# Kernel tuning notes

Hardware: AMD Instinct MI355X
Metric: run time of the kernel (lower is better)

The kernel has to match this reference:

```python
import jax, jax.numpy as jnp
import numpy as np
import math

B_GRAPHS = 256
L_NODES = 64
N_NODES = B_GRAPHS * L_NODES
N_EDGES = N_NODES * 4
HEADS = 8
D_INNER = 512
N_DAGS = 1
DIAMETER = 64


def setup_inputs() -> dict:
    key = jax.random.key(0)
    ks = jax.random.split(key, 8)
    x = jax.random.normal(ks[0], (N_NODES, D_INNER), jnp.float32)
    B = jax.random.normal(ks[1], (N_NODES, D_INNER), jnp.float32)
    C = jax.random.normal(ks[2], (N_NODES, D_INNER), jnp.float32)
    dt = jax.random.normal(ks[3], (N_NODES, N_DAGS * HEADS * 2), jnp.float32)
    dt_edge = jax.random.normal(ks[4], (N_EDGES, N_DAGS * HEADS), jnp.float32)
    # DAG edges: within each graph, src_local < dst_local (gap 1..7) -> strictly upper triangular
    u = jax.random.randint(ks[5], (N_EDGES,), 0, L_NODES - 1)
    gap = jax.random.randint(ks[6], (N_EDGES,), 1, 8)
    v = jnp.minimum(u + gap, L_NODES - 1)
    graph = jnp.arange(N_EDGES) // (N_EDGES // B_GRAPHS)
    edge_index = jnp.stack([graph * L_NODES + u, graph * L_NODES + v]).astype(jnp.int32)
    data_batch = (jnp.arange(N_NODES) // L_NODES).astype(jnp.int32)
    dag_masks = jnp.ones((N_DAGS, N_EDGES), jnp.float32)
    # dt_bias init as in module __init__ (inverse softplus of dt in [1e-3, 1e-1])
    rng = np.random.default_rng(0)
    dtv = np.exp(rng.uniform(size=(HEADS,)) * (math.log(0.1) - math.log(0.001)) + math.log(0.001))
    dtv = np.clip(dtv, 1e-4, None)
    dt_bias = jnp.asarray(dtv + np.log(-np.expm1(-dtv)), jnp.float32)
    D = jnp.ones((HEADS,), jnp.float32)
    return dict(x=x, B=B, C=C, dt=dt, dt_edge=dt_edge, dt_bias=dt_bias, D=D,
                dag_masks=dag_masks, edge_index=edge_index, data_batch=data_batch,
                diameter=DIAMETER)


def _repeated_squaring_inverse(A, diam):
    # (I - A)^{-1} = prod_k (I + A^{2^k}) for nilpotent A; O(log diam) matmuls
    j = 2 ** int(math.ceil(math.log2(diam)))
    I = jnp.eye(A.shape[-1], dtype=A.dtype)
    last = A
    M = I + A
    for _ in range(2, int(math.log2(j)) + 1):
        last = last @ last
        M = M @ (I + last)
    return M


def reference(x, B, C, dt, dt_edge, dt_bias, D, dag_masks, edge_index, data_batch, diameter):
    N, din = x.shape
    g, E = dag_masks.shape
    n = dt_bias.shape[0]
    b = int(data_batch[-1]) + 1
    l = N // b  # equal-size graphs -> dense batching is a reshape, mask all-True
    h = din // n
    src, dst = edge_index[0], edge_index[1]

    # dt_node: (N, g*n*c) -> (c, g, n, N); softplus(dt + bias)
    c = dt.shape[1] // (g * n)
    dtn = dt.reshape(N, g, n, c).transpose(3, 1, 2, 0)
    dtn = jax.nn.softplus(dtn + dt_bias[None, None, :, None])
    dte = dt_edge.reshape(E, g, n).transpose(1, 2, 0)  # (g,n,E)
    dte = jax.nn.softplus(dte + dt_bias[None, :, None])

    dt_s, dt_t = dtn[0], dtn[1]
    dt_sum = (dt_s[:, :, src] + dt_t[:, :, dst] + dte) / np.sqrt(3.0)  # (g,n,E)
    dt_exp = jnp.exp(-dt_sum)
    msk = dag_masks[:, None, :]
    dt_sum = dt_sum * msk
    dt_exp = dt_exp * msk

    # dense adjacency with per-edge attrs; note 'b l1 l2 (g n) -> b g n l2 l1' transpose
    b_e = src // l
    sl = src % l
    dl = dst % l
    attr = dt_exp.transpose(2, 0, 1).reshape(E, g * n)
    adj = jnp.zeros((b, l, l, g * n), x.dtype).at[b_e, sl, dl].add(attr)
    A = adj.reshape(b, l, l, g, n).transpose(0, 3, 4, 2, 1)  # (b,g,n,l,l)

    # normalize_mat: sqrt outer product of in-degree counts, clamped at 1
    ec = jnp.zeros((g, N), x.dtype).at[:, dst].add(dag_masks)
    ec_dense = ec.T.reshape(b, l, g)
    outer = jnp.sqrt(jnp.einsum('blg,btg->bglt', ec_dense, ec_dense))
    outer = jnp.where(outer < 1.0, 1.0, outer)
    A = A / outer[:, :, None]

    dnorm = jnp.zeros((g, n, N), x.dtype).at[:, :, dst].add(dt_sum)
    dnorm = dnorm.transpose(2, 0, 1).reshape(b, l, g, n).transpose(0, 2, 3, 1)  # (b,g,n,l)

    A2 = A.reshape(b, g * n, l, l).astype(jnp.float32)
    L = _repeated_squaring_inverse(A2, int(diameter))
    L = L.reshape(b, g, n, l, l) * dnorm[..., None]

    x4 = x.reshape(b, l, n, h).transpose(0, 2, 1, 3)  # (b,n,l,h)
    B3 = B.reshape(b, l, -1)
    C3 = C.reshape(b, l, -1)
    # y = einsum(C,L,B,x) with B/C broadcast over (g,n): fold C.B^T into L
    CB = jnp.einsum('bld,btd->blt', C3, B3)
    M = L * CB[:, None, None]
    y = jnp.einsum('bgnlt,bnth->bgnlh', M, x4)
    y = y + x4[:, None] * D[None, None, :, None, None]
    y = y.transpose(0, 3, 1, 2, 4).reshape(N, g, n * h)  # b g n l h -> (N, g, n*h)
    y = y.sum(axis=1) / np.sqrt(g)
    return y
```

## Files before the change

kernel.cpp:

```cpp
#include <hip/hip_runtime.h>
#include <math.h>

#define NGRAPH 256
#define LNODE  64
#define HEADS  8
#define DIN    512
#define EPG    256
#define NEDGE  65536

typedef short bf16x8 __attribute__((ext_vector_type(8)));
typedef float f32x4 __attribute__((ext_vector_type(4)));

__device__ __forceinline__ float softplusf(float v) {
    return (v > 20.f) ? v : log1pf(expf(v));
}
__device__ __forceinline__ unsigned short f2bf(float f) {
    union { float f; unsigned u; } c; c.f = f;
    unsigned r = c.u + 0x7fffu + ((c.u >> 16) & 1u);
    return (unsigned short)(r >> 16);
}
__device__ __forceinline__ float bf2f(unsigned short h) {
    union { float f; unsigned u; } c; c.u = ((unsigned)h) << 16;
    return c.f;
}

__global__ __launch_bounds__(256) void cb_kernel(const float* __restrict__ Bm,
                                                 const float* __restrict__ Cm,
                                                 float* __restrict__ CBp,
                                                 int dper, int tposed) {
    int b = blockIdx.x;
    int slice = blockIdx.y;
    __shared__ float Cs[64 * 68];
    __shared__ float Bs[64 * 68];
    int tid = threadIdx.x;
    int ti = tid >> 4, tj = tid & 15;
    float acc[4][4] = {};
    const float* Cg = Cm + (size_t)b * 64 * DIN;
    const float* Bg = Bm + (size_t)b * 64 * DIN;
    int d_lo = slice * dper;
    for (int d0 = d_lo; d0 < d_lo + dper; d0 += 64) {
        __syncthreads();
        #pragma unroll
        for (int k = 0; k < 4; ++k) {
            int f = k * 256 + tid;
            int row = f >> 4;
            int c4 = (f & 15) << 2;
            *(float4*)(Cs + row * 68 + c4) = *(const float4*)(Cg + row * DIN + d0 + c4);
            *(float4*)(Bs + row * 68 + c4) = *(const float4*)(Bg + row * DIN + d0 + c4);
        }
        __syncthreads();
        for (int d = 0; d < 64; d += 4) {
            float4 cr[4], br[4];
            #pragma unroll
            for (int r = 0; r < 4; ++r) cr[r] = *(const float4*)(Cs + (4 * ti + r) * 68 + d);
            #pragma unroll
            for (int c = 0; c < 4; ++c) br[c] = *(const float4*)(Bs + (4 * tj + c) * 68 + d);
            #pragma unroll
            for (int r = 0; r < 4; ++r)
                #pragma unroll
                for (int c = 0; c < 4; ++c)
                    acc[r][c] += cr[r].x * br[c].x + cr[r].y * br[c].y +
                                 cr[r].z * br[c].z + cr[r].w * br[c].w;
        }
    }
    float* outp = CBp + ((size_t)slice * NGRAPH + b) * 4096;
    if (!tposed) {
        #pragma unroll
        for (int r = 0; r < 4; ++r)
            *(float4*)(outp + (4 * ti + r) * 64 + 4 * tj) =
                make_float4(acc[r][0], acc[r][1], acc[r][2], acc[r][3]);
    } else {
        #pragma unroll
        for (int r = 0; r < 4; ++r)
            #pragma unroll
            for (int c = 0; c < 4; ++c)
                outp[(4 * tj + c) * 64 + (4 * ti + r)] = acc[r][c];
    }
}

__global__ __launch_bounds__(256, 4) void fused2_kernel(const float* __restrict__ x,
                                                        const float* __restrict__ dt,
                                                        const float* __restrict__ dt_edge,
                                                        const float* __restrict__ dt_bias,
                                                        const float* __restrict__ Dp,
                                                        const float* __restrict__ dag_masks,
                                                        const int* __restrict__ edge_index,
                                                        const float* __restrict__ CBp,
                                                        float* __restrict__ out,
                                                        int nslice) {
    int b = blockIdx.x;
    int head = blockIdx.y;
    __shared__ unsigned short CBsh[64 * 64];
    __shared__ unsigned short Wl[64 * 72];
    __shared__ unsigned short Xt[64 * 72];
    __shared__ float Ab[512];
    __shared__ float dnsh[64];
    __shared__ float ecsh[64];
    __shared__ float dts[64];
    __shared__ float dtt[64];
    int tid = threadIdx.x;
    int w = tid >> 6;
    int lane = tid & 63;

    for (int s4 = tid; s4 < 1024; s4 += 256) {
        float4 v = make_float4(0.f, 0.f, 0.f, 0.f);
        for (int s = 0; s < nslice; ++s) {
            float4 p = *(const float4*)(CBp + ((size_t)s * NGRAPH + b) * 4096 + s4 * 4);
            v.x += p.x; v.y += p.y; v.z += p.z; v.w += p.w;
        }
        unsigned short* q = &CBsh[s4 * 4];
        q[0] = f2bf(v.x); q[1] = f2bf(v.y); q[2] = f2bf(v.z); q[3] = f2bf(v.w);
    }
    const float* xg0 = x + (size_t)b * 64 * DIN + head * 64;
    #pragma unroll
    for (int k = 0; k < 4; ++k) {
        int s = k * 256 + tid;
        int t = s >> 4;
        int e0 = (s & 15) << 2;
        float4 v = *(const float4*)(xg0 + (size_t)t * DIN + e0);
        Xt[(e0 + 0) * 72 + t] = f2bf(v.x);
        Xt[(e0 + 1) * 72 + t] = f2bf(v.y);
        Xt[(e0 + 2) * 72 + t] = f2bf(v.z);
        Xt[(e0 + 3) * 72 + t] = f2bf(v.w);
    }
    for (int k = tid; k < 512; k += 256) Ab[k] = 0.f;
    float bias = dt_bias[head];
    if (tid < 64) {
        dnsh[tid] = 0.f;
        ecsh[tid] = 0.f;
        int node = b * 64 + tid;
        dts[tid] = softplusf(dt[node * 16 + head * 2 + 0] + bias);
        dtt[tid] = softplusf(dt[node * 16 + head * 2 + 1] + bias);
    }
    __syncthreads();

    {
        int e = b * EPG + tid;
        int sl = edge_index[e] & 63;
        int dl = edge_index[NEDGE + e] & 63;
        float mk = dag_masks[e];
        float de = softplusf(dt_edge[e * HEADS + head] + bias);
        float dsum = (dts[sl] + dtt[dl] + de) * 0.57735026918962576451f;
        float dexp = expf(-dsum);
        atomicAdd(&Ab[dl * 8 + (dl - sl)], dexp * mk);
        atomicAdd(&dnsh[dl], dsum * mk);
        atomicAdd(&ecsh[dl], mk);
    }
    __syncthreads();

    for (int k = tid; k < 512; k += 256) {
        int i = k >> 3, d = k & 7;
        int src = i - d;
        if (d >= 1 && src >= 0) {
            float den = sqrtf(ecsh[i] * ecsh[src]);
            if (den < 1.f) den = 1.f;
            Ab[k] = Ab[k] / den;
        }
    }
    __syncthreads();

    if (w == 0) {
        int j = lane;
        float Dh = Dp[head];
        float mwin[7] = {0.f, 0.f, 0.f, 0.f, 0.f, 0.f, 0.f};
        for (int i = 0; i < 64; ++i) {
            float mi = (j == i) ? 1.f : 0.f;
            #pragma unroll
            for (int s = 0; s < 7; ++s) mi += Ab[i * 8 + s + 1] * mwin[s];
            float wv = mi * bf2f(CBsh[i * 64 + j]) * dnsh[i];
            if (j == i) wv += Dh;
            Wl[i * 72 + j] = f2bf(wv);
            #pragma unroll
            for (int s = 6; s > 0; --s) mwin[s] = mwin[s - 1];
            mwin[0] = mi;
        }
    }
    __syncthreads();

    {
        int m = lane & 15;
        int quad = lane >> 4;
        bf16x8 a0 = *(const bf16x8*)(&Wl[(16 * w + m) * 72 + quad * 8]);
        bf16x8 a1 = *(const bf16x8*)(&Wl[(16 * w + m) * 72 + 32 + quad * 8]);
        float* og = out + ((size_t)b * 64) * DIN + head * 64;
        #pragma unroll
        for (int eb = 0; eb < 4; ++eb) {
            bf16x8 b0 = *(const bf16x8*)(&Xt[(eb * 16 + m) * 72 + quad * 8]);
            bf16x8 b1 = *(const bf16x8*)(&Xt[(eb * 16 + m) * 72 + 32 + quad * 8]);
            f32x4 acc = {0.f, 0.f, 0.f, 0.f};
            acc = __builtin_amdgcn_mfma_f32_16x16x32_bf16(a0, b0, acc, 0, 0, 0);
            acc = __builtin_amdgcn_mfma_f32_16x16x32_bf16(a1, b1, acc, 0, 0, 0);
            #pragma unroll
            for (int r = 0; r < 4; ++r) {
                int row = 16 * w + quad * 4 + r;
                og[(size_t)row * DIN + eb * 16 + m] = acc[r];
            }
        }
    }
}

__global__ __launch_bounds__(256, 4) void fused_kernel(const float* __restrict__ x,
                                                       const float* __restrict__ dt,
                                                       const float* __restrict__ dt_edge,
                                                       const float* __restrict__ dt_bias,
                                                       const float* __restrict__ Dp,
                                                       const float* __restrict__ dag_masks,
                                                       const int* __restrict__ edge_index,
                                                       const float* __restrict__ CBt,
                                                       float* __restrict__ out,
                                                       int nslice) {
    int b = blockIdx.x;
    int head = blockIdx.y;
    __shared__ float Ab[64 * 8];
    __shared__ float Mt[64 * 68];
    __shared__ float Xs[64 * 64];
    __shared__ float dnsh[64];
    __shared__ float ecsh[64];
    __shared__ float dts[64];
    __shared__ float dtt[64];
    int tid = threadIdx.x;

    int t4 = tid >> 2;
    int ib = (tid & 3) << 4;
    float4 cbsum[4];
    #pragma unroll
    for (int g = 0; g < 4; ++g) cbsum[g] = make_float4(0.f, 0.f, 0.f, 0.f);
    for (int s = 0; s < nslice; ++s) {
        const float* p = CBt + ((size_t)s * NGRAPH + b) * 4096 + t4 * 64 + ib;
        #pragma unroll
        for (int g = 0; g < 4; ++g) {
            float4 v = *(const float4*)(p + 4 * g);
            cbsum[g].x += v.x; cbsum[g].y += v.y; cbsum[g].z += v.z; cbsum[g].w += v.w;
        }
    }
    const float* xg0 = x + ((size_t)b * 64) * DIN + head * 64;
    #pragma unroll
    for (int k = 0; k < 4; ++k) {
        int s = k * 256 + tid;
        int row = s >> 4;
        int c4 = (s & 15) << 2;
        *(float4*)(Xs + row * 64 + c4) = *(const float4*)(xg0 + (size_t)row * DIN + c4);
    }
    for (int k = tid; k < 512; k += 256) Ab[k] = 0.f;
    float bias = dt_bias[head];
    if (tid < 64) {
        dnsh[tid] = 0.f;
        ecsh[tid] = 0.f;
        int node = b * 64 + tid;
        dts[tid] = softplusf(dt[node * 16 + head * 2 + 0] + bias);
        dtt[tid] = softplusf(dt[node * 16 + head * 2 + 1] + bias);
    }
    __syncthreads();
    {
        int e = b * EPG + tid;
        int sl = edge_index[e] & 63;
        int dl = edge_index[NEDGE + e] & 63;
        float mk = dag_masks[e];
        float de = softplusf(dt_edge[e * HEADS + head] + bias);
        float dsum = (dts[sl] + dtt[dl] + de) * 0.57735026918962576451f;
        float dexp = expf(-dsum);
        atomicAdd(&Ab[dl * 8 + (dl - sl)], dexp * mk);
        atomicAdd(&dnsh[dl], dsum * mk);
        atomicAdd(&ecsh[dl], mk);
    }
    __syncthreads();
    for (int k = tid; k < 512; k += 256) {
        int i = k >> 3, d = k & 7;
        int src = i - d;
        if (d >= 1 && src >= 0) {
            float den = sqrtf(ecsh[i] * ecsh[src]);
            if (den < 1.f) den = 1.f;
            Ab[k] = Ab[k] / den;
        }
    }
    __syncthreads();
    if (tid < 64) {
        int j = tid;
        float mwin[7] = {0.f, 0.f, 0.f, 0.f, 0.f, 0.f, 0.f};
        for (int i = 0; i < 64; ++i) {
            float mi = (j == i) ? 1.f : 0.f;
            #pragma unroll
            for (int s = 0; s < 7; ++s) mi += Ab[i * 8 + s + 1] * mwin[s];
            Mt[j * 65 + i] = mi;
            #pragma unroll
            for (int s = 6; s > 0; --s) mwin[s] = mwin[s - 1];
            mwin[0] = mi;
        }
    }
    __syncthreads();
    {
        float wv[16];
        #pragma unroll
        for (int g = 0; g < 4; ++g) {
            float4 dn4 = *(const float4*)(dnsh + ib + 4 * g);
            wv[4 * g + 0] = Mt[t4 * 65 + ib + 4 * g + 0] * cbsum[g].x * dn4.x;
            wv[4 * g + 1] = Mt[t4 * 65 + ib + 4 * g + 1] * cbsum[g].y * dn4.y;
            wv[4 * g + 2] = Mt[t4 * 65 + ib + 4 * g + 2] * cbsum[g].z * dn4.z;
            wv[4 * g + 3] = Mt[t4 * 65 + ib + 4 * g + 3] * cbsum[g].w * dn4.w;
        }
        __syncthreads();
        #pragma unroll
        for (int g = 0; g < 4; ++g)
            *(float4*)(Mt + t4 * 68 + ib + 4 * g) =
                make_float4(wv[4 * g + 0], wv[4 * g + 1], wv[4 * g + 2], wv[4 * g + 3]);
    }
    __syncthreads();
    int ti = tid >> 4, tj = tid & 15;
    float acc[4][4] = {};
    #pragma unroll 4
    for (int t = 0; t < 64; ++t) {
        float4 w4 = *(const float4*)(Mt + t * 68 + 4 * ti);
        float4 xv = *(const float4*)(Xs + t * 64 + 4 * tj);
        acc[0][0] += w4.x * xv.x; acc[0][1] += w4.x * xv.y; acc[0][2] += w4.x * xv.z; acc[0][3] += w4.x * xv.w;
        acc[1][0] += w4.y * xv.x; acc[1][1] += w4.y * xv.y; acc[1][2] += w4.y * xv.z; acc[1][3] += w4.y * xv.w;
        acc[2][0] += w4.z * xv.x; acc[2][1] += w4.z * xv.y; acc[2][2] += w4.z * xv.z; acc[2][3] += w4.z * xv.w;
        acc[3][0] += w4.w * xv.x; acc[3][1] += w4.w * xv.y; acc[3][2] += w4.w * xv.z; acc[3][3] += w4.w * xv.w;
    }
    float Dh = Dp[head];
    #pragma unroll
    for (int r = 0; r < 4; ++r) {
        int i = 4 * ti + r;
        float4 xres = *(const float4*)(Xs + i * 64 + 4 * tj);
        float4 v;
        v.x = acc[r][0] + xres.x * Dh;
        v.y = acc[r][1] + xres.y * Dh;
        v.z = acc[r][2] + xres.z * Dh;
        v.w = acc[r][3] + xres.w * Dh;
        *(float4*)(out + ((size_t)(b * 64 + i)) * DIN + head * 64 + 4 * tj) = v;
    }
}

extern "C" void kernel_launch(void* const* d_in, const int* in_sizes, int n_in,
                              void* d_out, int out_size, void* d_ws, size_t ws_size,
                              hipStream_t stream) {
    const float* x        = (const float*)d_in[0];
    const float* Bm       = (const float*)d_in[1];
    const float* Cm       = (const float*)d_in[2];
    const float* dt       = (const float*)d_in[3];
    const float* dt_edge  = (const float*)d_in[4];
    const float* dt_bias  = (const float*)d_in[5];
    const float* Dp       = (const float*)d_in[6];
    const float* dag_mask = (const float*)d_in[7];
    const int*   edge_idx = (const int*)d_in[8];
    float* out = (float*)d_out;

    const size_t CBSLICE = (size_t)NGRAPH * 4096 * 4;
    float* CBp = (float*)d_ws;

    if (ws_size >= 2 * CBSLICE) {
        int nslice = 2;
        cb_kernel<<<dim3(NGRAPH, nslice), 256, 0, stream>>>(Bm, Cm, CBp, DIN / nslice, 0);
        fused2_kernel<<<dim3(NGRAPH, HEADS), 256, 0, stream>>>(x, dt, dt_edge, dt_bias, Dp,
                                                               dag_mask, edge_idx, CBp, out, nslice);
    } else {
        int nslice = 1;
        cb_kernel<<<dim3(NGRAPH, nslice), 256, 0, stream>>>(Bm, Cm, CBp, DIN / nslice, 1);
        fused_kernel<<<dim3(NGRAPH, HEADS), 256, 0, stream>>>(x, dt, dt_edge, dt_bias, Dp,
                                                              dag_mask, edge_idx, CBp, out, nslice);
    }
}
```

Measured before the change: 193.4 us.

## Fuse CB product and all heads into one per-graph kernel with MFMA

Replaces the two-kernel pipeline (CB partial products in workspace, then a per-(graph, head) kernel) with a single kernel per graph where 8 waves each handle one head. C·B^T is computed in-kernel with bf16 MFMA using a hi/lo split for near-fp32 accuracy, which removes the workspace round-trip and the separate launch. It also shares in-degree counts across heads, swizzles the LDS layouts for Xt/Wl to avoid bank conflicts, and compacts the Ab band storage. The cost is a large LDS footprint and only 256 blocks of 512 threads, which may limit occupancy and latency hiding.

```diff
diff --git a/kernel.cpp b/kernel.cpp
--- a/kernel.cpp
+++ b/kernel.cpp
@@ -2,7 +2,6 @@
 #include <math.h>
 
 #define NGRAPH 256
-#define LNODE  64
 #define HEADS  8
 #define DIN    512
 #define EPG    256
@@ -23,339 +22,202 @@
     union { float f; unsigned u; } c; c.u = ((unsigned)h) << 16;
     return c.f;
 }
-
-__global__ __launch_bounds__(256) void cb_kernel(const float* __restrict__ Bm,
-                                                 const float* __restrict__ Cm,
-                                                 float* __restrict__ CBp,
-                                                 int dper, int tposed) {
-    int b = blockIdx.x;
-    int slice = blockIdx.y;
-    __shared__ float Cs[64 * 68];
-    __shared__ float Bs[64 * 68];
-    int tid = threadIdx.x;
-    int ti = tid >> 4, tj = tid & 15;
-    float acc[4][4] = {};
-    const float* Cg = Cm + (size_t)b * 64 * DIN;
-    const float* Bg = Bm + (size_t)b * 64 * DIN;
-    int d_lo = slice * dper;
-    for (int d0 = d_lo; d0 < d_lo + dper; d0 += 64) {
-        __syncthreads();
-        #pragma unroll
-        for (int k = 0; k < 4; ++k) {
-            int f = k * 256 + tid;
-            int row = f >> 4;
-            int c4 = (f & 15) << 2;
-            *(float4*)(Cs + row * 68 + c4) = *(const float4*)(Cg + row * DIN + d0 + c4);
-            *(float4*)(Bs + row * 68 + c4) = *(const float4*)(Bg + row * DIN + d0 + c4);
-        }
-        __syncthreads();
-        for (int d = 0; d < 64; d += 4) {
-            float4 cr[4], br[4];
+__device__ __forceinline__ int swz_idx(int row, int t) {
+    int g = ((t >> 3) ^ (row ^ (row >> 3))) & 7;
+    return (row << 6) | (g << 3) | (t & 7);
+}
+__device__ __forceinline__ void loadsplit(const float* p, bf16x8& hi, bf16x8& lo) {
+    float4 u = *(const float4*)p;
+    float4 v = *(const float4*)(p + 4);
+    float vv[8] = {u.x, u.y, u.z, u.w, v.x, v.y, v.z, v.w};
+    #pragma unroll
+    for (int j = 0; j < 8; ++j) {
+        union { float f; unsigned q; } c; c.f = vv[j];
+        unsigned hb = c.q & 0xffff0000u;
+        hi[j] = (short)(unsigned short)(hb >> 16);
+        union { float f; unsigned q; } d; d.q = hb;
+        union { float f; unsigned q; } e2; e2.f = vv[j] - d.f;
+        lo[j] = (short)(unsigned short)(e2.q >> 16);
+    }
+}
+
+__global__ __launch_bounds__(512, 2) void dag_fused_kernel(
+        const float* __restrict__ x,
+        const float* __restrict__ Bm,
+        const float* __restrict__ Cm,
+        const float* __restrict__ dt,
+        const float* __restrict__ dt_edge,
+        const float* __restrict__ dt_bias,
+        const float* __restrict__ Dp,
+        const float* __restrict__ dag_masks,
+        const int* __restrict__ edge_index,
+        float* __restrict__ out) {
+    __shared__ unsigned short CBsh[64 * 68];
+    __shared__ __align__(16) unsigned short Xt[HEADS][4096];
+    __shared__ __align__(16) unsigned short Wl[HEADS][4096];
+    __shared__ float Ab[HEADS][448];
+    __shared__ float dts[HEADS][64];
+    __shared__ float dtt[HEADS][64];
+    __shared__ float dnsh[HEADS][64];
+    __shared__ float ecsh[64];
+
+    const int b = blockIdx.x;
+    const int tid = threadIdx.x;
+    const int w = tid >> 6;
+    const int lane = tid & 63;
+    const int lm = lane & 15;
+    const int quad = lane >> 4;
+    const float bias = dt_bias[w];
+
+    {
+        float2 dv = *(const float2*)(dt + ((size_t)(b * 64 + lane)) * 16 + w * 2);
+        dts[w][lane] = softplusf(dv.x + bias);
+        dtt[w][lane] = softplusf(dv.y + bias);
+        dnsh[w][lane] = 0.f;
+        #pragma unroll
+        for (int s = 0; s < 7; ++s) Ab[w][lane * 7 + s] = 0.f;
+        if (w == 0) ecsh[lane] = 0.f;
+    }
+    __syncthreads();
+
+    if (tid < EPG) {
+        int e = b * EPG + tid;
+        atomicAdd(&ecsh[edge_index[NEDGE + e] & 63], dag_masks[e]);
+    }
+    {
+        const int mi = w >> 1;
+        const int ni0 = (w & 1) * 2;
+        const float* Cr = Cm + ((size_t)(b * 64 + mi * 16 + lm)) * DIN + quad * 8;
+        const float* B0 = Bm + ((size_t)(b * 64 + ni0 * 16 + lm)) * DIN + quad * 8;
+        const float* B1 = B0 + (size_t)16 * DIN;
+        f32x4 acc0 = {0.f, 0.f, 0.f, 0.f};
+        f32x4 acc1 = {0.f, 0.f, 0.f, 0.f};
+        #pragma unroll 4
+        for (int ks = 0; ks < 16; ++ks) {
+            bf16x8 ah, al, b0h, b0l, b1h, b1l;
+            loadsplit(Cr + ks * 32, ah, al);
+            loadsplit(B0 + ks * 32, b0h, b0l);
+            loadsplit(B1 + ks * 32, b1h, b1l);
+            acc0 = __builtin_amdgcn_mfma_f32_16x16x32_bf16(ah, b0h, acc0, 0, 0, 0);
+            acc0 = __builtin_amdgcn_mfma_f32_16x16x32_bf16(ah, b0l, acc0, 0, 0, 0);
+            acc0 = __builtin_amdgcn_mfma_f32_16x16x32_bf16(al, b0h, acc0, 0, 0, 0);
+            acc1 = __builtin_amdgcn_mfma_f32_16x16x32_bf16(ah, b1h, acc1, 0, 0, 0);
+            acc1 = __builtin_amdgcn_mfma_f32_16x16x32_bf16(ah, b1l, acc1, 0, 0, 0);
+            acc1 = __builtin_amdgcn_mfma_f32_16x16x32_bf16(al, b1h, acc1, 0, 0, 0);
+        }
+        #pragma unroll
+        for (int r = 0; r < 4; ++r) {
+            int row = mi * 16 + quad * 4 + r;
+            CBsh[row * 68 + ni0 * 16 + lm] = f2bf(acc0[r]);
+            CBsh[row * 68 + (ni0 + 1) * 16 + lm] = f2bf(acc1[r]);
+        }
+    }
+    {
+        const float* xg = x + (size_t)b * 64 * DIN + w * 64;
+        #pragma unroll 4
+        for (int r = 0; r < 16; ++r) {
+            int t = r * 4 + quad;
+            int e0 = lm * 4;
+            float4 v = *(const float4*)(xg + (size_t)t * DIN + e0);
+            Xt[w][swz_idx(e0 + 0, t)] = f2bf(v.x);
+            Xt[w][swz_idx(e0 + 1, t)] = f2bf(v.y);
+            Xt[w][swz_idx(e0 + 2, t)] = f2bf(v.z);
+            Xt[w][swz_idx(e0 + 3, t)] = f2bf(v.w);
+        }
+    }
+    __syncthreads();
+
+    {
+        #pragma unroll
+        for (int eo = 0; eo < 4; ++eo) {
+            int e = b * EPG + eo * 64 + lane;
+            int sl = edge_index[e] & 63;
+            int dl = edge_index[NEDGE + e] & 63;
+            float mk = dag_masks[e];
+            float de = softplusf(dt_edge[(size_t)e * HEADS + w] + bias);
+            float dsum = (dts[w][sl] + dtt[w][dl] + de) * 0.57735026918962576451f;
+            float dexp = expf(-dsum);
+            atomicAdd(&Ab[w][dl * 7 + (dl - sl - 1)], dexp * mk);
+            atomicAdd(&dnsh[w][dl], dsum * mk);
+        }
+    }
+    __syncthreads();
+
+    {
+        float eci = ecsh[lane];
+        #pragma unroll
+        for (int s = 0; s < 7; ++s) {
+            int src = lane - 1 - s;
+            if (src >= 0) {
+                float den = sqrtf(eci * ecsh[src]);
+                if (den < 1.f) den = 1.f;
+                Ab[w][lane * 7 + s] = Ab[w][lane * 7 + s] / den;
+            }
+        }
+    }
+    __syncthreads();
+
+    {
+        const int j = lane;
+        const float Dh = Dp[w];
+        float mwin[7] = {0.f, 0.f, 0.f, 0.f, 0.f, 0.f, 0.f};
+        const float* abp = &Ab[w][0];
+        for (int i = 0; i < 64; ++i) {
+            float mi_ = (j == i) ? 1.f : 0.f;
             #pragma unroll
-            for (int r = 0; r < 4; ++r) cr[r] = *(const float4*)(Cs + (4 * ti + r) * 68 + d);
-            #pragma unroll
-            for (int c = 0; c < 4; ++c) br[c] = *(const float4*)(Bs + (4 * tj + c) * 68 + d);
-            #pragma unroll
-            for (int r = 0; r < 4; ++r)
-                #pragma unroll
-                for (int c = 0; c < 4; ++c)
-                    acc[r][c] += cr[r].x * br[c].x + cr[r].y * br[c].y +
-                                 cr[r].z * br[c].z + cr[r].w * br[c].w;
-        }
-    }
-    float* outp = CBp + ((size_t)slice * NGRAPH + b) * 4096;
-    if (!tposed) {
-        #pragma unroll
-        for (int r = 0; r < 4; ++r)
-            *(float4*)(outp + (4 * ti + r) * 64 + 4 * tj) =
-                make_float4(acc[r][0], acc[r][1], acc[r][2], acc[r][3]);
-    } else {
-        #pragma unroll
-        for (int r = 0; r < 4; ++r)
-            #pragma unroll
-            for (int c = 0; c < 4; ++c)
-                outp[(4 * tj + c) * 64 + (4 * ti + r)] = acc[r][c];
-    }
-}
-
-__global__ __launch_bounds__(256, 4) void fused2_kernel(const float* __restrict__ x,
-                                                        const float* __restrict__ dt,
-                                                        const float* __restrict__ dt_edge,
-                                                        const float* __restrict__ dt_bias,
-                                                        const float* __restrict__ Dp,
-                                                        const float* __restrict__ dag_masks,
-                                                        const int* __restrict__ edge_index,
-                                                        const float* __restrict__ CBp,
-                                                        float* __restrict__ out,
-                                                        int nslice) {
-    int b = blockIdx.x;
-    int head = blockIdx.y;
-    __shared__ unsigned short CBsh[64 * 64];
-    __shared__ unsigned short Wl[64 * 72];
-    __shared__ unsigned short Xt[64 * 72];
-    __shared__ float Ab[512];
-    __shared__ float dnsh[64];
-    __shared__ float ecsh[64];
-    __shared__ float dts[64];
-    __shared__ float dtt[64];
-    int tid = threadIdx.x;
-    int w = tid >> 6;
-    int lane = tid & 63;
-
-    for (int s4 = tid; s4 < 1024; s4 += 256) {
-        float4 v = make_float4(0.f, 0.f, 0.f, 0.f);
-        for (int s = 0; s < nslice; ++s) {
-            float4 p = *(const float4*)(CBp + ((size_t)s * NGRAPH + b) * 4096 + s4 * 4);
-            v.x += p.x; v.y += p.y; v.z += p.z; v.w += p.w;
-        }
-        unsigned short* q = &CBsh[s4 * 4];
-        q[0] = f2bf(v.x); q[1] = f2bf(v.y); q[2] = f2bf(v.z); q[3] = f2bf(v.w);
-    }
-    const float* xg0 = x + (size_t)b * 64 * DIN + head * 64;
-    #pragma unroll
-    for (int k = 0; k < 4; ++k) {
-        int s = k * 256 + tid;
-        int t = s >> 4;
-        int e0 = (s & 15) << 2;
-        float4 v = *(const float4*)(xg0 + (size_t)t * DIN + e0);
-        Xt[(e0 + 0) * 72 + t] = f2bf(v.x);
-        Xt[(e0 + 1) * 72 + t] = f2bf(v.y);
-        Xt[(e0 + 2) * 72 + t] = f2bf(v.z);
-        Xt[(e0 + 3) * 72 + t] = f2bf(v.w);
-    }
-    for (int k = tid; k < 512; k += 256) Ab[k] = 0.f;
-    float bias = dt_bias[head];
-    if (tid < 64) {
-        dnsh[tid] = 0.f;
-        ecsh[tid] = 0.f;
-        int node = b * 64 + tid;
-        dts[tid] = softplusf(dt[node * 16 + head * 2 + 0] + bias);
-        dtt[tid] = softplusf(dt[node * 16 + head * 2 + 1] + bias);
-    }
-    __syncthreads();
-
-    {
-        int e = b * EPG + tid;
-        int sl = edge_index[e] & 63;
-        int dl = edge_index[NEDGE + e] & 63;
-        float mk = dag_masks[e];
-        float de = softplusf(dt_edge[e * HEADS + head] + bias);
-        float dsum = (dts[sl] + dtt[dl] + de) * 0.57735026918962576451f;
-        float dexp = expf(-dsum);
-        atomicAdd(&Ab[dl * 8 + (dl - sl)], dexp * mk);
-        atomicAdd(&dnsh[dl], dsum * mk);
-        atomicAdd(&ecsh[dl], mk);
-    }
-    __syncthreads();
-
-    for (int k = tid; k < 512; k += 256) {
-        int i = k >> 3, d = k & 7;
-        int src = i - d;
-        if (d >= 1 && src >= 0) {
-            float den = sqrtf(ecsh[i] * ecsh[src]);
-            if (den < 1.f) den = 1.f;
-            Ab[k] = Ab[k] / den;
-        }
-    }
-    __syncthreads();
-
-    if (w == 0) {
-        int j = lane;
-        float Dh = Dp[head];
-        float mwin[7] = {0.f, 0.f, 0.f, 0.f, 0.f, 0.f, 0.f};
-        for (int i = 0; i < 64; ++i) {
-            float mi = (j == i) ? 1.f : 0.f;
-            #pragma unroll
-            for (int s = 0; s < 7; ++s) mi += Ab[i * 8 + s + 1] * mwin[s];
-            float wv = mi * bf2f(CBsh[i * 64 + j]) * dnsh[i];
+            for (int s = 0; s < 7; ++s) mi_ += abp[i * 7 + s] * mwin[s];
+            float wv = mi_ * bf2f(CBsh[i * 68 + j]) * dnsh[w][i];
             if (j == i) wv += Dh;
-            Wl[i * 72 + j] = f2bf(wv);
+            Wl[w][swz_idx(i, j)] = f2bf(wv);
             #pragma unroll
             for (int s = 6; s > 0; --s) mwin[s] = mwin[s - 1];
-            mwin[0] = mi;
-        }
-    }
-    __syncthreads();
-
-    {
-        int m = lane & 15;
-        int quad = lane >> 4;
-        bf16x8 a0 = *(const bf16x8*)(&Wl[(16 * w + m) * 72 + quad * 8]);
-        bf16x8 a1 = *(const bf16x8*)(&Wl[(16 * w + m) * 72 + 32 + quad * 8]);
-        float* og = out + ((size_t)b * 64) * DIN + head * 64;
+            mwin[0] = mi_;
+        }
+    }
+    __syncthreads();
+
+    {
+        bf16x8 af[4][2];
+        #pragma unroll
+        for (int mi = 0; mi < 4; ++mi) {
+            int row0 = mi * 16 + lm;
+            af[mi][0] = *(const bf16x8*)(&Wl[w][swz_idx(row0, quad * 8)]);
+            af[mi][1] = *(const bf16x8*)(&Wl[w][swz_idx(row0, 32 + quad * 8)]);
+        }
+        float* og = out + (size_t)b * 64 * DIN + w * 64;
         #pragma unroll
         for (int eb = 0; eb < 4; ++eb) {
-            bf16x8 b0 = *(const bf16x8*)(&Xt[(eb * 16 + m) * 72 + quad * 8]);
-            bf16x8 b1 = *(const bf16x8*)(&Xt[(eb * 16 + m) * 72 + 32 + quad * 8]);
-            f32x4 acc = {0.f, 0.f, 0.f, 0.f};
-            acc = __builtin_amdgcn_mfma_f32_16x16x32_bf16(a0, b0, acc, 0, 0, 0);
-            acc = __builtin_amdgcn_mfma_f32_16x16x32_bf16(a1, b1, acc, 0, 0, 0);
+            int er = eb * 16 + lm;
+            bf16x8 b0 = *(const bf16x8*)(&Xt[w][swz_idx(er, quad * 8)]);
+            bf16x8 b1 = *(const bf16x8*)(&Xt[w][swz_idx(er, 32 + quad * 8)]);
             #pragma unroll
-            for (int r = 0; r < 4; ++r) {
-                int row = 16 * w + quad * 4 + r;
-                og[(size_t)row * DIN + eb * 16 + m] = acc[r];
+            for (int mi = 0; mi < 4; ++mi) {
+                f32x4 acc = {0.f, 0.f, 0.f, 0.f};
+                acc = __builtin_amdgcn_mfma_f32_16x16x32_bf16(af[mi][0], b0, acc, 0, 0, 0);
+                acc = __builtin_amdgcn_mfma_f32_16x16x32_bf16(af[mi][1], b1, acc, 0, 0, 0);
+                #pragma unroll
+                for (int r = 0; r < 4; ++r) {
+                    int row = mi * 16 + quad * 4 + r;
+                    og[(size_t)row * DIN + eb * 16 + lm] = acc[r];
+                }
             }
         }
-    }
-}
-
-__global__ __launch_bounds__(256, 4) void fused_kernel(const float* __restrict__ x,
-                                                       const float* __restrict__ dt,
-                                                       const float* __restrict__ dt_edge,
-                                                       const float* __restrict__ dt_bias,
-                                                       const float* __restrict__ Dp,
-                                                       const float* __restrict__ dag_masks,
-                                                       const int* __restrict__ edge_index,
-                                                       const float* __restrict__ CBt,
-                                                       float* __restrict__ out,
-                                                       int nslice) {
-    int b = blockIdx.x;
-    int head = blockIdx.y;
-    __shared__ float Ab[64 * 8];
-    __shared__ float Mt[64 * 68];
-    __shared__ float Xs[64 * 64];
-    __shared__ float dnsh[64];
-    __shared__ float ecsh[64];
-    __shared__ float dts[64];
-    __shared__ float dtt[64];
-    int tid = threadIdx.x;
-
-    int t4 = tid >> 2;
-    int ib = (tid & 3) << 4;
-    float4 cbsum[4];
-    #pragma unroll
-    for (int g = 0; g < 4; ++g) cbsum[g] = make_float4(0.f, 0.f, 0.f, 0.f);
-    for (int s = 0; s < nslice; ++s) {
-        const float* p = CBt + ((size_t)s * NGRAPH + b) * 4096 + t4 * 64 + ib;
-        #pragma unroll
-        for (int g = 0; g < 4; ++g) {
-            float4 v = *(const float4*)(p + 4 * g);
-            cbsum[g].x += v.x; cbsum[g].y += v.y; cbsum[g].z += v.z; cbsum[g].w += v.w;
-        }
-    }
-    const float* xg0 = x + ((size_t)b * 64) * DIN + head * 64;
-    #pragma unroll
-    for (int k = 0; k < 4; ++k) {
-        int s = k * 256 + tid;
-        int row = s >> 4;
-        int c4 = (s & 15) << 2;
-        *(float4*)(Xs + row * 64 + c4) = *(const float4*)(xg0 + (size_t)row * DIN + c4);
-    }
-    for (int k = tid; k < 512; k += 256) Ab[k] = 0.f;
-    float bias = dt_bias[head];
-    if (tid < 64) {
-        dnsh[tid] = 0.f;
-        ecsh[tid] = 0.f;
-        int node = b * 64 + tid;
-        dts[tid] = softplusf(dt[node * 16 + head * 2 + 0] + bias);
-        dtt[tid] = softplusf(dt[node * 16 + head * 2 + 1] + bias);
-    }
-    __syncthreads();
-    {
-        int e = b * EPG + tid;
-        int sl = edge_index[e] & 63;
-        int dl = edge_index[NEDGE + e] & 63;
-        float mk = dag_masks[e];
-        float de = softplusf(dt_edge[e * HEADS + head] + bias);
-        float dsum = (dts[sl] + dtt[dl] + de) * 0.57735026918962576451f;
-        float dexp = expf(-dsum);
-        atomicAdd(&Ab[dl * 8 + (dl - sl)], dexp * mk);
-        atomicAdd(&dnsh[dl], dsum * mk);
-        atomicAdd(&ecsh[dl], mk);
-    }
-    __syncthreads();
-    for (int k = tid; k < 512; k += 256) {
-        int i = k >> 3, d = k & 7;
-        int src = i - d;
-        if (d >= 1 && src >= 0) {
-            float den = sqrtf(ecsh[i] * ecsh[src]);
-            if (den < 1.f) den = 1.f;
-            Ab[k] = Ab[k] / den;
-        }
-    }
-    __syncthreads();
-    if (tid < 64) {
-        int j = tid;
-        float mwin[7] = {0.f, 0.f, 0.f, 0.f, 0.f, 0.f, 0.f};
-        for (int i = 0; i < 64; ++i) {
-            float mi = (j == i) ? 1.f : 0.f;
-            #pragma unroll
-            for (int s = 0; s < 7; ++s) mi += Ab[i * 8 + s + 1] * mwin[s];
-            Mt[j * 65 + i] = mi;
-            #pragma unroll
-            for (int s = 6; s > 0; --s) mwin[s] = mwin[s - 1];
-            mwin[0] = mi;
-        }
-    }
-    __syncthreads();
-    {
-        float wv[16];
-        #pragma unroll
-        for (int g = 0; g < 4; ++g) {
-            float4 dn4 = *(const float4*)(dnsh + ib + 4 * g);
-            wv[4 * g + 0] = Mt[t4 * 65 + ib + 4 * g + 0] * cbsum[g].x * dn4.x;
-            wv[4 * g + 1] = Mt[t4 * 65 + ib + 4 * g + 1] * cbsum[g].y * dn4.y;
-            wv[4 * g + 2] = Mt[t4 * 65 + ib + 4 * g + 2] * cbsum[g].z * dn4.z;
-            wv[4 * g + 3] = Mt[t4 * 65 + ib + 4 * g + 3] * cbsum[g].w * dn4.w;
-        }
-        __syncthreads();
-        #pragma unroll
-        for (int g = 0; g < 4; ++g)
-            *(float4*)(Mt + t4 * 68 + ib + 4 * g) =
-                make_float4(wv[4 * g + 0], wv[4 * g + 1], wv[4 * g + 2], wv[4 * g + 3]);
-    }
-    __syncthreads();
-    int ti = tid >> 4, tj = tid & 15;
-    float acc[4][4] = {};
-    #pragma unroll 4
-    for (int t = 0; t < 64; ++t) {
-        float4 w4 = *(const float4*)(Mt + t * 68 + 4 * ti);
-        float4 xv = *(const float4*)(Xs + t * 64 + 4 * tj);
-        acc[0][0] += w4.x * xv.x; acc[0][1] += w4.x * xv.y; acc[0][2] += w4.x * xv.z; acc[0][3] += w4.x * xv.w;
-        acc[1][0] += w4.y * xv.x; acc[1][1] += w4.y * xv.y; acc[1][2] += w4.y * xv.z; acc[1][3] += w4.y * xv.w;
-        acc[2][0] += w4.z * xv.x; acc[2][1] += w4.z * xv.y; acc[2][2] += w4.z * xv.z; acc[2][3] += w4.z * xv.w;
-        acc[3][0] += w4.w * xv.x; acc[3][1] += w4.w * xv.y; acc[3][2] += w4.w * xv.z; acc[3][3] += w4.w * xv.w;
-    }
-    float Dh = Dp[head];
-    #pragma unroll
-    for (int r = 0; r < 4; ++r) {
-        int i = 4 * ti + r;
-        float4 xres = *(const float4*)(Xs + i * 64 + 4 * tj);
-        float4 v;
-        v.x = acc[r][0] + xres.x * Dh;
-        v.y = acc[r][1] + xres.y * Dh;
-        v.z = acc[r][2] + xres.z * Dh;
-        v.w = acc[r][3] + xres.w * Dh;
-        *(float4*)(out + ((size_t)(b * 64 + i)) * DIN + head * 64 + 4 * tj) = v;
     }
 }
 
 extern "C" void kernel_launch(void* const* d_in, const int* in_sizes, int n_in,
                               void* d_out, int out_size, void* d_ws, size_t ws_size,
                               hipStream_t stream) {
-    const float* x        = (const float*)d_in[0];
-    const float* Bm       = (const float*)d_in[1];
-    const float* Cm       = (const float*)d_in[2];
-    const float* dt       = (const float*)d_in[3];
-    const float* dt_edge  = (const float*)d_in[4];
-    const float* dt_bias  = (const float*)d_in[5];
-    const float* Dp       = (const float*)d_in[6];
-    const float* dag_mask = (const float*)d_in[7];
-    const int*   edge_idx = (const int*)d_in[8];
-    float* out = (float*)d_out;
-
-    const size_t CBSLICE = (size_t)NGRAPH * 4096 * 4;
-    float* CBp = (float*)d_ws;
-
-    if (ws_size >= 2 * CBSLICE) {
-        int nslice = 2;
-        cb_kernel<<<dim3(NGRAPH, nslice), 256, 0, stream>>>(Bm, Cm, CBp, DIN / nslice, 0);
-        fused2_kernel<<<dim3(NGRAPH, HEADS), 256, 0, stream>>>(x, dt, dt_edge, dt_bias, Dp,
-                                                               dag_mask, edge_idx, CBp, out, nslice);
-    } else {
-        int nslice = 1;
-        cb_kernel<<<dim3(NGRAPH, nslice), 256, 0, stream>>>(Bm, Cm, CBp, DIN / nslice, 1);
-        fused_kernel<<<dim3(NGRAPH, HEADS), 256, 0, stream>>>(x, dt, dt_edge, dt_bias, Dp,
-                                                              dag_mask, edge_idx, CBp, out, nslice);
-    }
-}
+    (void)in_sizes; (void)n_in; (void)out_size; (void)d_ws; (void)ws_size;
+    dag_fused_kernel<<<dim3(NGRAPH), dim3(512), 0, stream>>>(
+        (const float*)d_in[0],
+        (const float*)d_in[1],
+        (const float*)d_in[2],
+        (const float*)d_in[3],
+        (const float*)d_in[4],
+        (const float*)d_in[5],
+        (const float*)d_in[6],
+        (const float*)d_in[7],
+        (const int*)d_in[8],
+        (float*)d_out);
+}
```

New measurement: 169.9 us. 12.2% less time.
